# Kernel tuning notes

Hardware: AMD Instinct MI355X
Metric: run time of the kernel (lower is better)

The kernel has to match this reference:

```python
import jax, jax.numpy as jnp
import numpy as np


def setup_inputs() -> dict:
    key = jax.random.key(0)
    ks = jax.random.split(key, 4)
    B, C, T = 4, 256, 4096
    Cq = C // 8
    x = jax.random.normal(ks[0], (B, C, T), dtype=jnp.float32)
    Wq = jax.random.normal(ks[1], (Cq, C), dtype=jnp.float32) * (1.0 / np.sqrt(C))
    Wk = jax.random.normal(ks[2], (Cq, C), dtype=jnp.float32) * (1.0 / np.sqrt(C))
    Wv = jax.random.normal(ks[3], (C, C), dtype=jnp.float32) * (1.0 / np.sqrt(C))
    bq = jnp.zeros((Cq,), dtype=jnp.float32)
    bk = jnp.zeros((Cq,), dtype=jnp.float32)
    bv = jnp.zeros((C,), dtype=jnp.float32)
    return {"x": x, "Wq": Wq, "bq": bq, "Wk": Wk, "bk": bk, "Wv": Wv, "bv": bv}


def reference(x, Wq, bq, Wk, bk, Wv, bv):
    # x: [B, C, T]; 1x1 conv == per-timestep linear over channels
    q = jnp.einsum('oc,bct->bto', Wq, x) + bq          # [B, T, Cq]  (proj_query permuted)
    k = jnp.einsum('oc,bct->bot', Wk, x) + bk[:, None]  # [B, Cq, T]
    v = jnp.einsum('oc,bct->bot', Wv, x) + bv[:, None]  # [B, C, T]
    attn = jax.nn.softmax(jnp.einsum('bto,bos->bts', q, k), axis=-1)  # [B, T, T]
    out = jnp.einsum('bcs,bts->bct', v, attn)           # V @ attn^T
    return out + x
```

## Files before the change

kernel.cpp:

```cpp
#include <hip/hip_runtime.h>
#include <hip/hip_bf16.h>

#define BB 4
#define CC 256
#define TT 4096
#define CQ 32
#define LOG2E 1.44269504088896340736f

typedef __bf16 bf16;
typedef __bf16 bf16x4 __attribute__((ext_vector_type(4)));
typedef __bf16 bf16x8 __attribute__((ext_vector_type(8)));
typedef float floatx4 __attribute__((ext_vector_type(4)));

#define MFMA16(a, b, c) __builtin_amdgcn_mfma_f32_16x16x32_bf16(a, b, c, 0, 0, 0)

__device__ __forceinline__ void lgkm_barrier() {
    asm volatile("s_waitcnt lgkmcnt(0)" ::: "memory");
    __builtin_amdgcn_s_barrier();
    asm volatile("" ::: "memory");
}

__global__ __launch_bounds__(256) void wconv_kernel(
    const float* __restrict__ Wq, const float* __restrict__ Wk,
    const float* __restrict__ Wv, bf16* __restrict__ Wf)
{
    int gid = blockIdx.x * 256 + threadIdx.x;
    int o   = gid >> 5;
    int c8  = gid & 31;
    const float* src;
    if (o < 32)       src = Wq + (size_t)o * CC;
    else if (o < 64)  src = Wk + (size_t)(o - 32) * CC;
    else              src = Wv + (size_t)(o - 64) * CC;
    float4 a = *(const float4*)(src + c8 * 8);
    float4 b = *(const float4*)(src + c8 * 8 + 4);
    bf16x8 v;
    v[0] = (bf16)a.x; v[1] = (bf16)a.y; v[2] = (bf16)a.z; v[3] = (bf16)a.w;
    v[4] = (bf16)b.x; v[5] = (bf16)b.y; v[6] = (bf16)b.z; v[7] = (bf16)b.w;
    int j = o >> 4, l15 = o & 15;
    int k = c8 >> 2, quad = c8 & 3;
    *(bf16x8*)(Wf + ((size_t)((j * 8 + k) * 4 + quad) * 16 + l15) * 8) = v;
}

__global__ __launch_bounds__(256) void xtproj_kernel(
    const float* __restrict__ x, const bf16* __restrict__ Wf,
    const float* __restrict__ bq, const float* __restrict__ bk,
    const float* __restrict__ bv,
    bf16* __restrict__ Qo, bf16* __restrict__ Ko, bf16* __restrict__ Vo)
{
    __shared__ float sf[64][33];
    __shared__ bf16  xbf[32][256];
    __shared__ __align__(16) bf16 Vl[256][40];

    const int tid  = threadIdx.x;
    const int lane = tid & 63, w = tid >> 6;
    const int l15  = lane & 15, quad = lane >> 4;
    const int bx   = blockIdx.x, b = blockIdx.y;
    const int t0   = bx * 32;

    for (int cc = 0; cc < 4; ++cc) {
        #pragma unroll
        for (int p = 0; p < 2; ++p) {
            int cl = p * 32 + (tid >> 3);
            int t4 = (tid & 7) * 4;
            float4 v = *(const float4*)(
                x + ((size_t)(b * CC + cc * 64 + cl)) * TT + t0 + t4);
            sf[cl][t4 + 0] = v.x; sf[cl][t4 + 1] = v.y;
            sf[cl][t4 + 2] = v.z; sf[cl][t4 + 3] = v.w;
        }
        __syncthreads();
        {
            int tl = tid >> 3;
            int c8 = (tid & 7) * 8;
            bf16x8 o;
            #pragma unroll
            for (int j = 0; j < 8; ++j) o[j] = (bf16)sf[c8 + j][tl];
            int chunk = cc * 8 + ((tid & 7) ^ (tl & 7));
            *(bf16x8*)(&xbf[tl][0] + chunk * 8) = o;
        }
        __syncthreads();
    }

    const int h  = w >> 1;
    const int tl = (w & 1) * 16 + l15;
    const int t  = t0 + tl;

    const bf16* wfb = Wf + ((size_t)(h * 10) * 8 * 4 + quad) * 16 * 8 + l15 * 8;

    floatx4 acc[10] = {};
    for (int k = 0; k < 8; ++k) {
        int chunk = (k * 4 + quad) ^ (tl & 7);
        bf16x8 xf = *(const bf16x8*)(&xbf[tl][0] + chunk * 8);
        #pragma unroll
        for (int j = 0; j < 10; ++j) {
            bf16x8 a = *(const bf16x8*)(wfb + ((size_t)(j * 8 + k) * 4) * 128);
            acc[j] = MFMA16(a, xf, acc[j]);
        }
    }

    if (h == 0) {
        #pragma unroll
        for (int mt = 0; mt < 2; ++mt) {
            float4 bsq = *(const float4*)(bq + mt * 16 + quad * 4);
            float4 bsk = *(const float4*)(bk + mt * 16 + quad * 4);
            bf16x4 vq, vk;
            vq[0] = (bf16)((acc[mt][0] + bsq.x) * LOG2E);
            vq[1] = (bf16)((acc[mt][1] + bsq.y) * LOG2E);
            vq[2] = (bf16)((acc[mt][2] + bsq.z) * LOG2E);
            vq[3] = (bf16)((acc[mt][3] + bsq.w) * LOG2E);
            vk[0] = (bf16)(acc[2 + mt][0] + bsk.x);
            vk[1] = (bf16)(acc[2 + mt][1] + bsk.y);
            vk[2] = (bf16)(acc[2 + mt][2] + bsk.z);
            vk[3] = (bf16)(acc[2 + mt][3] + bsk.w);
            *(bf16x4*)(Qo + ((size_t)(b * TT + t)) * CQ + mt * 16 + quad * 4) = vq;
            *(bf16x4*)(Ko + ((size_t)(b * TT + t)) * CQ + mt * 16 + quad * 4) = vk;
        }
        #pragma unroll
        for (int vm = 0; vm < 6; ++vm) {
            float4 bs = *(const float4*)(bv + vm * 16 + quad * 4);
            #pragma unroll
            for (int r = 0; r < 4; ++r)
                Vl[vm * 16 + quad * 4 + r][tl] =
                    (bf16)(acc[4 + vm][r] + ((const float*)&bs)[r]);
        }
    } else {
        #pragma unroll
        for (int i = 0; i < 10; ++i) {
            int vm = 6 + i;
            float4 bs = *(const float4*)(bv + vm * 16 + quad * 4);
            #pragma unroll
            for (int r = 0; r < 4; ++r)
                Vl[vm * 16 + quad * 4 + r][tl] =
                    (bf16)(acc[i][r] + ((const float*)&bs)[r]);
        }
    }
    __syncthreads();

    #pragma unroll
    for (int g = 0; g < 4; ++g) {
        int c = tid;
        bf16x8 v = *(const bf16x8*)(&Vl[c][g * 8]);
        *(bf16x8*)(Vo + ((size_t)(b * 512 + (t0 >> 3) + g) * 256 + c) * 8) = v;
    }
}

__global__ __launch_bounds__(256, 2) void flash_kernel(
    const bf16* __restrict__ Q, const bf16* __restrict__ K,
    const bf16* __restrict__ Vf, float* __restrict__ Op, float* __restrict__ lp)
{
    __shared__ __align__(16) char Ps[16384];

    const int fid  = blockIdx.x;
    const int xcd  = fid & 7;
    const int sp   = xcd & 1, b = xcd >> 1;
    const int t0   = (fid >> 3) * 64;

    const int tid  = threadIdx.x;
    const int lane = tid & 63, w = tid >> 6;
    const int l15  = lane & 15, quad = lane >> 4;
    const size_t sbase = (size_t)sp * (TT / 2);

    const bf16x8 qf = *(const bf16x8*)(
        Q + ((size_t)b * TT + t0 + w * 16 + l15) * CQ + quad * 8);

    const bf16* Kb = K + ((size_t)b * TT + sbase) * CQ;

    const bf16* Vfb = Vf + ((size_t)(b * 512 + sp * 256 + quad) * 256 +
                            w * 64 + l15) * 8;

    floatx4 acc[4][4] = {};
    float lsum[4] = {};
    const int prow = w * 16 + quad * 4;

    bf16x8 kfc[4];
    #pragma unroll
    for (int nt = 0; nt < 4; ++nt)
        kfc[nt] = *(const bf16x8*)(Kb + (size_t)(nt * 16 + l15) * CQ + quad * 8);

    for (int st = 0; st < 32; ++st) {
        const unsigned pb = (unsigned)(st & 1) * 8192u;

        bf16x8 vf[2][4];
        #pragma unroll
        for (int kt = 0; kt < 2; ++kt)
            #pragma unroll
            for (int ntc = 0; ntc < 4; ++ntc)
                vf[kt][ntc] = *(const bf16x8*)(
                    Vfb + ((size_t)(st * 8 + kt * 4) * 256 + ntc * 16) * 8);

        floatx4 sc[4];
        #pragma unroll
        for (int nt = 0; nt < 4; ++nt) {
            floatx4 z = {};
            sc[nt] = MFMA16(qf, kfc[nt], z);
        }

        #pragma unroll
        for (int nt = 0; nt < 4; ++nt)
            #pragma unroll
            for (int r = 0; r < 4; ++r) {
                float pv = __builtin_amdgcn_exp2f(sc[nt][r]);
                lsum[r] += pv;
                int row  = prow + r;
                int s    = nt * 16 + l15;
                int slot = (s >> 3) ^ (row & 7);
                *(bf16*)(Ps + pb + row * 128 + slot * 16 + (s & 7) * 2) = (bf16)pv;
            }

        if (st + 1 < 32) {
            #pragma unroll
            for (int nt = 0; nt < 4; ++nt)
                kfc[nt] = *(const bf16x8*)(
                    Kb + (size_t)((st + 1) * 64 + nt * 16 + l15) * CQ + quad * 8);
        }

        lgkm_barrier();

        bf16x8 pa[4][2];
        #pragma unroll
        for (int mt = 0; mt < 4; ++mt) {
            int row = mt * 16 + l15;
            #pragma unroll
            for (int kt = 0; kt < 2; ++kt) {
                int slot = (kt * 4 + quad) ^ (row & 7);
                pa[mt][kt] = *(const bf16x8*)(Ps + pb + row * 128 + slot * 16);
            }
        }

        __builtin_amdgcn_s_setprio(1);
        #pragma unroll
        for (int kt = 0; kt < 2; ++kt)
            #pragma unroll
            for (int ntc = 0; ntc < 4; ++ntc)
                #pragma unroll
                for (int mt = 0; mt < 4; ++mt)
                    acc[mt][ntc] = MFMA16(pa[mt][kt], vf[kt][ntc], acc[mt][ntc]);
        __builtin_amdgcn_s_setprio(0);
    }

    #pragma unroll
    for (int r = 0; r < 4; ++r) {
        float s = lsum[r];
        s += __shfl_xor(s, 1); s += __shfl_xor(s, 2);
        s += __shfl_xor(s, 4); s += __shfl_xor(s, 8);
        lsum[r] = s;
    }

    float* op = Op + ((size_t)((sp * BB + b) * TT + t0)) * CC;
    #pragma unroll
    for (int mt = 0; mt < 4; ++mt)
        #pragma unroll
        for (int ntc = 0; ntc < 4; ++ntc)
            #pragma unroll
            for (int r = 0; r < 4; ++r)
                op[(size_t)(mt * 16 + quad * 4 + r) * CC + w * 64 + ntc * 16 + l15] =
                    acc[mt][ntc][r];
    if (l15 == 0) {
        #pragma unroll
        for (int r = 0; r < 4; ++r)
            lp[(size_t)(sp * BB + b) * TT + t0 + w * 16 + quad * 4 + r] = lsum[r];
    }
}

__global__ __launch_bounds__(256) void combine_kernel(
    const float* __restrict__ Op, const float* __restrict__ lp,
    const float* __restrict__ x, float* __restrict__ out)
{
    __shared__ float Os[32 * 260];
    __shared__ float Ls[32];
    const int tid = threadIdx.x;
    const int t0 = blockIdx.x * 32, b = blockIdx.y;

    if (tid < 32) {
        float l = lp[(size_t)b * TT + t0 + tid] + lp[(size_t)(BB + b) * TT + t0 + tid];
        Ls[tid] = 1.f / l;
    }
    const float* p0 = Op + ((size_t)(b * TT + t0)) * CC;
    const float* p1 = Op + ((size_t)((BB + b) * TT + t0)) * CC;
    #pragma unroll
    for (int it = 0; it < 8; ++it) {
        int chunk = it * 256 + tid;
        int t = chunk >> 6, c4 = (chunk & 63) * 4;
        float4 a = *(const float4*)(p0 + (size_t)t * CC + c4);
        float4 c2 = *(const float4*)(p1 + (size_t)t * CC + c4);
        Os[t * 260 + c4 + 0] = a.x + c2.x;
        Os[t * 260 + c4 + 1] = a.y + c2.y;
        Os[t * 260 + c4 + 2] = a.z + c2.z;
        Os[t * 260 + c4 + 3] = a.w + c2.w;
    }
    __syncthreads();

    const int tq = (tid & 7) * 4, crow = tid >> 3;
    #pragma unroll
    for (int pass = 0; pass < 8; ++pass) {
        int c = pass * 32 + crow;
        size_t base = ((size_t)(b * CC + c)) * TT + t0 + tq;
        float4 xr = *(const float4*)(x + base);
        float4 o;
        o.x = Os[(tq + 0) * 260 + c] * Ls[tq + 0] + xr.x;
        o.y = Os[(tq + 1) * 260 + c] * Ls[tq + 1] + xr.y;
        o.z = Os[(tq + 2) * 260 + c] * Ls[tq + 2] + xr.z;
        o.w = Os[(tq + 3) * 260 + c] * Ls[tq + 3] + xr.w;
        *(float4*)(out + base) = o;
    }
}

extern "C" void kernel_launch(void* const* d_in, const int* in_sizes, int n_in,
                              void* d_out, int out_size, void* d_ws, size_t ws_size,
                              hipStream_t stream) {
    const float* x  = (const float*)d_in[0];
    const float* Wq = (const float*)d_in[1];
    const float* bq = (const float*)d_in[2];
    const float* Wk = (const float*)d_in[3];
    const float* bk = (const float*)d_in[4];
    const float* Wv = (const float*)d_in[5];
    const float* bv = (const float*)d_in[6];
    float* out = (float*)d_out;

    char* ws = (char*)d_ws;
    bf16*  Wf = (bf16*)ws;
    bf16*  Qw = (bf16*)(ws + 163840);
    bf16*  Kw = (bf16*)(ws + 163840 + 1048576);
    bf16*  Vw = (bf16*)(ws + 163840 + 2097152);
    char*  R  = ws + 163840 + 2097152 + 8388608;
    float* Op = (float*)R;
    float* lp = (float*)(R + 33554432);

    wconv_kernel<<<dim3(40), 256, 0, stream>>>(Wq, Wk, Wv, Wf);
    xtproj_kernel<<<dim3(128, BB), 256, 0, stream>>>(x, Wf, bq, bk, bv, Qw, Kw, Vw);
    flash_kernel<<<dim3(512), 256, 0, stream>>>(Qw, Kw, Vw, Op, lp);
    combine_kernel<<<dim3(128, BB), 256, 0, stream>>>(Op, lp, x, out);
}
```

Baseline: 140.2 us.

## Fuse combine into flash kernel by splitting key columns across waves

Each block now covers 32 query rows over the full key range instead of 64 rows over half the keys. The four waves split into two row halves and two key-column halves for QK^T, then share P through LDS for the PV product. Row sums are reduced in LDS, and the epilogue normalises, adds the residual x and writes the output directly. This removes the fp32 partial-output buffers, the extra combine launch and its global traffic, at the cost of each block reading all of V rather than half of it.

```diff
diff --git a/kernel.cpp b/kernel.cpp
--- a/kernel.cpp
+++ b/kernel.cpp
@@ -145,39 +145,41 @@
 
 __global__ __launch_bounds__(256, 2) void flash_kernel(
     const bf16* __restrict__ Q, const bf16* __restrict__ K,
-    const bf16* __restrict__ Vf, float* __restrict__ Op, float* __restrict__ lp)
+    const bf16* __restrict__ Vf, const float* __restrict__ x,
+    float* __restrict__ out)
 {
-    __shared__ __align__(16) char Ps[16384];
+    __shared__ __align__(16) char Ps[8192];
+    __shared__ float lred[2][32];
 
     const int fid  = blockIdx.x;
-    const int xcd  = fid & 7;
-    const int sp   = xcd & 1, b = xcd >> 1;
-    const int t0   = (fid >> 3) * 64;
+    const int b    = (fid & 7) >> 1;
+    const int th   = fid & 1;
+    const int t0   = ((fid >> 3) + th * 64) * 32;
 
     const int tid  = threadIdx.x;
     const int lane = tid & 63, w = tid >> 6;
     const int l15  = lane & 15, quad = lane >> 4;
-    const size_t sbase = (size_t)sp * (TT / 2);
+    const int rw   = w & 1, sh = w >> 1;
 
     const bf16x8 qf = *(const bf16x8*)(
-        Q + ((size_t)b * TT + t0 + w * 16 + l15) * CQ + quad * 8);
-
-    const bf16* Kb = K + ((size_t)b * TT + sbase) * CQ;
-
-    const bf16* Vfb = Vf + ((size_t)(b * 512 + sp * 256 + quad) * 256 +
-                            w * 64 + l15) * 8;
-
-    floatx4 acc[4][4] = {};
+        Q + ((size_t)b * TT + t0 + rw * 16 + l15) * CQ + quad * 8);
+
+    const bf16* Kb = K + (size_t)b * TT * CQ;
+
+    const bf16* Vfb = Vf + ((size_t)(b * 512 + quad) * 256 + w * 64 + l15) * 8;
+
+    floatx4 acc[2][4] = {};
     float lsum[4] = {};
-    const int prow = w * 16 + quad * 4;
-
-    bf16x8 kfc[4];
-    #pragma unroll
-    for (int nt = 0; nt < 4; ++nt)
-        kfc[nt] = *(const bf16x8*)(Kb + (size_t)(nt * 16 + l15) * CQ + quad * 8);
-
-    for (int st = 0; st < 32; ++st) {
-        const unsigned pb = (unsigned)(st & 1) * 8192u;
+    const int prow = rw * 16 + quad * 4;
+
+    bf16x8 kfc[2];
+    #pragma unroll
+    for (int ntl = 0; ntl < 2; ++ntl)
+        kfc[ntl] = *(const bf16x8*)(
+            Kb + (size_t)((sh * 2 + ntl) * 16 + l15) * CQ + quad * 8);
+
+    for (int st = 0; st < 64; ++st) {
+        const unsigned pb = (unsigned)(st & 1) * 4096u;
 
         bf16x8 vf[2][4];
         #pragma unroll
@@ -187,37 +189,38 @@
                 vf[kt][ntc] = *(const bf16x8*)(
                     Vfb + ((size_t)(st * 8 + kt * 4) * 256 + ntc * 16) * 8);
 
-        floatx4 sc[4];
-        #pragma unroll
-        for (int nt = 0; nt < 4; ++nt) {
+        floatx4 sc[2];
+        #pragma unroll
+        for (int ntl = 0; ntl < 2; ++ntl) {
             floatx4 z = {};
-            sc[nt] = MFMA16(qf, kfc[nt], z);
-        }
-
-        #pragma unroll
-        for (int nt = 0; nt < 4; ++nt)
+            sc[ntl] = MFMA16(qf, kfc[ntl], z);
+        }
+
+        #pragma unroll
+        for (int ntl = 0; ntl < 2; ++ntl)
             #pragma unroll
             for (int r = 0; r < 4; ++r) {
-                float pv = __builtin_amdgcn_exp2f(sc[nt][r]);
+                float pv = __builtin_amdgcn_exp2f(sc[ntl][r]);
                 lsum[r] += pv;
                 int row  = prow + r;
-                int s    = nt * 16 + l15;
+                int s    = (sh * 2 + ntl) * 16 + l15;
                 int slot = (s >> 3) ^ (row & 7);
                 *(bf16*)(Ps + pb + row * 128 + slot * 16 + (s & 7) * 2) = (bf16)pv;
             }
 
-        if (st + 1 < 32) {
-            #pragma unroll
-            for (int nt = 0; nt < 4; ++nt)
-                kfc[nt] = *(const bf16x8*)(
-                    Kb + (size_t)((st + 1) * 64 + nt * 16 + l15) * CQ + quad * 8);
+        if (st + 1 < 64) {
+            #pragma unroll
+            for (int ntl = 0; ntl < 2; ++ntl)
+                kfc[ntl] = *(const bf16x8*)(
+                    Kb + (size_t)((st + 1) * 64 + (sh * 2 + ntl) * 16 + l15) * CQ
+                       + quad * 8);
         }
 
         lgkm_barrier();
 
-        bf16x8 pa[4][2];
-        #pragma unroll
-        for (int mt = 0; mt < 4; ++mt) {
+        bf16x8 pa[2][2];
+        #pragma unroll
+        for (int mt = 0; mt < 2; ++mt) {
             int row = mt * 16 + l15;
             #pragma unroll
             for (int kt = 0; kt < 2; ++kt) {
@@ -232,7 +235,7 @@
             #pragma unroll
             for (int ntc = 0; ntc < 4; ++ntc)
                 #pragma unroll
-                for (int mt = 0; mt < 4; ++mt)
+                for (int mt = 0; mt < 2; ++mt)
                     acc[mt][ntc] = MFMA16(pa[mt][kt], vf[kt][ntc], acc[mt][ntc]);
         __builtin_amdgcn_s_setprio(0);
     }
@@ -244,64 +247,36 @@
         s += __shfl_xor(s, 4); s += __shfl_xor(s, 8);
         lsum[r] = s;
     }
-
-    float* op = Op + ((size_t)((sp * BB + b) * TT + t0)) * CC;
-    #pragma unroll
-    for (int mt = 0; mt < 4; ++mt)
-        #pragma unroll
-        for (int ntc = 0; ntc < 4; ++ntc)
-            #pragma unroll
-            for (int r = 0; r < 4; ++r)
-                op[(size_t)(mt * 16 + quad * 4 + r) * CC + w * 64 + ntc * 16 + l15] =
-                    acc[mt][ntc][r];
     if (l15 == 0) {
         #pragma unroll
         for (int r = 0; r < 4; ++r)
-            lp[(size_t)(sp * BB + b) * TT + t0 + w * 16 + quad * 4 + r] = lsum[r];
-    }
-}
-
-__global__ __launch_bounds__(256) void combine_kernel(
-    const float* __restrict__ Op, const float* __restrict__ lp,
-    const float* __restrict__ x, float* __restrict__ out)
-{
-    __shared__ float Os[32 * 260];
-    __shared__ float Ls[32];
-    const int tid = threadIdx.x;
-    const int t0 = blockIdx.x * 32, b = blockIdx.y;
-
-    if (tid < 32) {
-        float l = lp[(size_t)b * TT + t0 + tid] + lp[(size_t)(BB + b) * TT + t0 + tid];
-        Ls[tid] = 1.f / l;
-    }
-    const float* p0 = Op + ((size_t)(b * TT + t0)) * CC;
-    const float* p1 = Op + ((size_t)((BB + b) * TT + t0)) * CC;
-    #pragma unroll
-    for (int it = 0; it < 8; ++it) {
-        int chunk = it * 256 + tid;
-        int t = chunk >> 6, c4 = (chunk & 63) * 4;
-        float4 a = *(const float4*)(p0 + (size_t)t * CC + c4);
-        float4 c2 = *(const float4*)(p1 + (size_t)t * CC + c4);
-        Os[t * 260 + c4 + 0] = a.x + c2.x;
-        Os[t * 260 + c4 + 1] = a.y + c2.y;
-        Os[t * 260 + c4 + 2] = a.z + c2.z;
-        Os[t * 260 + c4 + 3] = a.w + c2.w;
+            lred[sh][prow + r] = lsum[r];
     }
     __syncthreads();
 
-    const int tq = (tid & 7) * 4, crow = tid >> 3;
-    #pragma unroll
-    for (int pass = 0; pass < 8; ++pass) {
-        int c = pass * 32 + crow;
-        size_t base = ((size_t)(b * CC + c)) * TT + t0 + tq;
-        float4 xr = *(const float4*)(x + base);
-        float4 o;
-        o.x = Os[(tq + 0) * 260 + c] * Ls[tq + 0] + xr.x;
-        o.y = Os[(tq + 1) * 260 + c] * Ls[tq + 1] + xr.y;
-        o.z = Os[(tq + 2) * 260 + c] * Ls[tq + 2] + xr.z;
-        o.w = Os[(tq + 3) * 260 + c] * Ls[tq + 3] + xr.w;
-        *(float4*)(out + base) = o;
-    }
+    float linv[2][4];
+    #pragma unroll
+    for (int mt = 0; mt < 2; ++mt)
+        #pragma unroll
+        for (int r = 0; r < 4; ++r) {
+            int row = mt * 16 + quad * 4 + r;
+            linv[mt][r] = 1.f / (lred[0][row] + lred[1][row]);
+        }
+
+    #pragma unroll
+    for (int mt = 0; mt < 2; ++mt)
+        #pragma unroll
+        for (int ntc = 0; ntc < 4; ++ntc) {
+            int c = w * 64 + ntc * 16 + l15;
+            size_t base = ((size_t)(b * CC + c)) * TT + t0 + mt * 16 + quad * 4;
+            float4 xr = *(const float4*)(x + base);
+            float4 o;
+            o.x = acc[mt][ntc][0] * linv[mt][0] + xr.x;
+            o.y = acc[mt][ntc][1] * linv[mt][1] + xr.y;
+            o.z = acc[mt][ntc][2] * linv[mt][2] + xr.z;
+            o.w = acc[mt][ntc][3] * linv[mt][3] + xr.w;
+            *(float4*)(out + base) = o;
+        }
 }
 
 extern "C" void kernel_launch(void* const* d_in, const int* in_sizes, int n_in,
@@ -321,12 +296,8 @@
     bf16*  Qw = (bf16*)(ws + 163840);
     bf16*  Kw = (bf16*)(ws + 163840 + 1048576);
     bf16*  Vw = (bf16*)(ws + 163840 + 2097152);
-    char*  R  = ws + 163840 + 2097152 + 8388608;
-    float* Op = (float*)R;
-    float* lp = (float*)(R + 33554432);
 
     wconv_kernel<<<dim3(40), 256, 0, stream>>>(Wq, Wk, Wv, Wf);
     xtproj_kernel<<<dim3(128, BB), 256, 0, stream>>>(x, Wf, bq, bk, bv, Qw, Kw, Vw);
-    flash_kernel<<<dim3(512), 256, 0, stream>>>(Qw, Kw, Vw, Op, lp);
-    combine_kernel<<<dim3(128, BB), 256, 0, stream>>>(Op, lp, x, out);
-}
+    flash_kernel<<<dim3(512), 256, 0, stream>>>(Qw, Kw, Vw, x, out);
+}
```

Result: slower. 148.0 us (+5.6%).

## Halve flash query tile to 32 rows and double grid for occupancy

Applied to the files above, without the earlier changes.

The flash kernel now processes 32 query rows per block instead of 64 and launches twice as many blocks. The four waves split as two row groups times two key-column halves when computing scores, and the row sums are combined through shared memory. This shrinks registers and LDS per block to raise occupancy and the number of blocks in flight on the GPU. In exchange, each block re-reads the full V and K stream for half as many rows, which doubles global V traffic, and it adds a final block barrier.

```diff
diff --git a/kernel.cpp b/kernel.cpp
--- a/kernel.cpp
+++ b/kernel.cpp
@@ -143,41 +143,44 @@
     }
 }
 
-__global__ __launch_bounds__(256, 2) void flash_kernel(
+__global__ __launch_bounds__(256) void flash_kernel(
     const bf16* __restrict__ Q, const bf16* __restrict__ K,
     const bf16* __restrict__ Vf, float* __restrict__ Op, float* __restrict__ lp)
 {
-    __shared__ __align__(16) char Ps[16384];
+    __shared__ __align__(16) char Ps[8192];
+    __shared__ float lred[2][32];
 
     const int fid  = blockIdx.x;
     const int xcd  = fid & 7;
     const int sp   = xcd & 1, b = xcd >> 1;
-    const int t0   = (fid >> 3) * 64;
+    const int t0   = (fid >> 3) * 32;
 
     const int tid  = threadIdx.x;
     const int lane = tid & 63, w = tid >> 6;
     const int l15  = lane & 15, quad = lane >> 4;
+    const int rw   = w & 1, sh = w >> 1;
     const size_t sbase = (size_t)sp * (TT / 2);
 
     const bf16x8 qf = *(const bf16x8*)(
-        Q + ((size_t)b * TT + t0 + w * 16 + l15) * CQ + quad * 8);
+        Q + ((size_t)b * TT + t0 + rw * 16 + l15) * CQ + quad * 8);
 
     const bf16* Kb = K + ((size_t)b * TT + sbase) * CQ;
 
     const bf16* Vfb = Vf + ((size_t)(b * 512 + sp * 256 + quad) * 256 +
                             w * 64 + l15) * 8;
 
-    floatx4 acc[4][4] = {};
+    floatx4 acc[2][4] = {};
     float lsum[4] = {};
-    const int prow = w * 16 + quad * 4;
-
-    bf16x8 kfc[4];
-    #pragma unroll
-    for (int nt = 0; nt < 4; ++nt)
-        kfc[nt] = *(const bf16x8*)(Kb + (size_t)(nt * 16 + l15) * CQ + quad * 8);
+    const int prow = rw * 16 + quad * 4;
+
+    bf16x8 kfc[2];
+    #pragma unroll
+    for (int ntl = 0; ntl < 2; ++ntl)
+        kfc[ntl] = *(const bf16x8*)(
+            Kb + (size_t)((sh * 2 + ntl) * 16 + l15) * CQ + quad * 8);
 
     for (int st = 0; st < 32; ++st) {
-        const unsigned pb = (unsigned)(st & 1) * 8192u;
+        const unsigned pb = (unsigned)(st & 1) * 4096u;
 
         bf16x8 vf[2][4];
         #pragma unroll
@@ -187,37 +190,38 @@
                 vf[kt][ntc] = *(const bf16x8*)(
                     Vfb + ((size_t)(st * 8 + kt * 4) * 256 + ntc * 16) * 8);
 
-        floatx4 sc[4];
-        #pragma unroll
-        for (int nt = 0; nt < 4; ++nt) {
+        floatx4 sc[2];
+        #pragma unroll
+        for (int ntl = 0; ntl < 2; ++ntl) {
             floatx4 z = {};
-            sc[nt] = MFMA16(qf, kfc[nt], z);
-        }
-
-        #pragma unroll
-        for (int nt = 0; nt < 4; ++nt)
+            sc[ntl] = MFMA16(qf, kfc[ntl], z);
+        }
+
+        #pragma unroll
+        for (int ntl = 0; ntl < 2; ++ntl)
             #pragma unroll
             for (int r = 0; r < 4; ++r) {
-                float pv = __builtin_amdgcn_exp2f(sc[nt][r]);
+                float pv = __builtin_amdgcn_exp2f(sc[ntl][r]);
                 lsum[r] += pv;
                 int row  = prow + r;
-                int s    = nt * 16 + l15;
+                int s    = (sh * 2 + ntl) * 16 + l15;
                 int slot = (s >> 3) ^ (row & 7);
                 *(bf16*)(Ps + pb + row * 128 + slot * 16 + (s & 7) * 2) = (bf16)pv;
             }
 
         if (st + 1 < 32) {
             #pragma unroll
-            for (int nt = 0; nt < 4; ++nt)
-                kfc[nt] = *(const bf16x8*)(
-                    Kb + (size_t)((st + 1) * 64 + nt * 16 + l15) * CQ + quad * 8);
+            for (int ntl = 0; ntl < 2; ++ntl)
+                kfc[ntl] = *(const bf16x8*)(
+                    Kb + (size_t)((st + 1) * 64 + (sh * 2 + ntl) * 16 + l15) * CQ
+                       + quad * 8);
         }
 
         lgkm_barrier();
 
-        bf16x8 pa[4][2];
-        #pragma unroll
-        for (int mt = 0; mt < 4; ++mt) {
+        bf16x8 pa[2][2];
+        #pragma unroll
+        for (int mt = 0; mt < 2; ++mt) {
             int row = mt * 16 + l15;
             #pragma unroll
             for (int kt = 0; kt < 2; ++kt) {
@@ -232,7 +236,7 @@
             #pragma unroll
             for (int ntc = 0; ntc < 4; ++ntc)
                 #pragma unroll
-                for (int mt = 0; mt < 4; ++mt)
+                for (int mt = 0; mt < 2; ++mt)
                     acc[mt][ntc] = MFMA16(pa[mt][kt], vf[kt][ntc], acc[mt][ntc]);
         __builtin_amdgcn_s_setprio(0);
     }
@@ -244,21 +248,24 @@
         s += __shfl_xor(s, 4); s += __shfl_xor(s, 8);
         lsum[r] = s;
     }
+    if (l15 == 0) {
+        #pragma unroll
+        for (int r = 0; r < 4; ++r)
+            lred[sh][prow + r] = lsum[r];
+    }
+    __syncthreads();
+    if (tid < 32)
+        lp[(size_t)(sp * BB + b) * TT + t0 + tid] = lred[0][tid] + lred[1][tid];
 
     float* op = Op + ((size_t)((sp * BB + b) * TT + t0)) * CC;
     #pragma unroll
-    for (int mt = 0; mt < 4; ++mt)
+    for (int mt = 0; mt < 2; ++mt)
         #pragma unroll
         for (int ntc = 0; ntc < 4; ++ntc)
             #pragma unroll
             for (int r = 0; r < 4; ++r)
                 op[(size_t)(mt * 16 + quad * 4 + r) * CC + w * 64 + ntc * 16 + l15] =
                     acc[mt][ntc][r];
-    if (l15 == 0) {
-        #pragma unroll
-        for (int r = 0; r < 4; ++r)
-            lp[(size_t)(sp * BB + b) * TT + t0 + w * 16 + quad * 4 + r] = lsum[r];
-    }
 }
 
 __global__ __launch_bounds__(256) void combine_kernel(
@@ -327,6 +334,6 @@
 
     wconv_kernel<<<dim3(40), 256, 0, stream>>>(Wq, Wk, Wv, Wf);
     xtproj_kernel<<<dim3(128, BB), 256, 0, stream>>>(x, Wf, bq, bk, bv, Qw, Kw, Vw);
-    flash_kernel<<<dim3(512), 256, 0, stream>>>(Qw, Kw, Vw, Op, lp);
+    flash_kernel<<<dim3(1024), 256, 0, stream>>>(Qw, Kw, Vw, Op, lp);
     combine_kernel<<<dim3(128, BB), 256, 0, stream>>>(Op, lp, x, out);
 }
```

After: 156.5 us. 11.6% more time.
